# Performance work log

Measured on AMD Instinct MI355X. Metric: run time of the kernel, lower is better.

Reference implementation:

```python
import jax, jax.numpy as jnp
import numpy as np


def setup_inputs() -> dict:
    key = jax.random.key(0)
    k1, k2 = jax.random.split(key)
    x = jax.random.normal(k1, (16, 4096, 256), dtype=jnp.float32)
    embedding = jax.random.normal(k2, (1024, 256), dtype=jnp.float32)
    return {"x": x, "embedding": embedding}


def reference(x, embedding):
    # which_dim = -1 (default): no permute.
    shape = x.shape
    xf = x.reshape(-1, shape[-1])  # [N, D]
    x_sq = jnp.sum(xf * xf, axis=-1, keepdims=True)          # [N, 1]
    e_sq = jnp.sum(embedding * embedding, axis=-1)           # [K]
    dist = -(x_sq - 2.0 * (xf @ embedding.T) + e_sq[None, :])  # [N, K]
    embed_indices = jnp.argmax(dist, axis=1)                 # [N]
    embed_indices = embed_indices.reshape(shape[:-1])        # [B, S]
    quantization = embedding[embed_indices]                  # [B, S, D]
    return (quantization, embed_indices)
```

## Files before the change

### kernel.cpp

```cpp
#include <hip/hip_runtime.h>
#include <hip/hip_fp16.h>
#include <math.h>

#define MROWS   65536
#define NCODES  1024
#define KD      256
#define MARGIN  0.25f

typedef unsigned short u16;
typedef __attribute__((ext_vector_type(8))) _Float16 hfrag;
typedef __attribute__((ext_vector_type(4))) float f32x4;

#define IOFF ((size_t)MROWS * KD)

__device__ __forceinline__ float addrn(float a, float b) {
    float d; asm("v_add_f32 %0, %1, %2" : "=v"(d) : "v"(a), "v"(b)); return d;
}

__device__ __forceinline__ float sumsq_vf8ic4(const float* __restrict__ xr) {
    float a[4][8];
#pragma unroll
    for (int i = 0; i < 4; ++i)
#pragma unroll
        for (int l = 0; l < 8; ++l) a[i][l] = 0.f;
#pragma unroll
    for (int m = 0; m < 8; ++m)
#pragma unroll
        for (int i = 0; i < 4; ++i)
#pragma unroll
            for (int l = 0; l < 8; ++l) {
                float v = xr[m * 32 + i * 8 + l];
                a[i][l] = fmaf(v, v, a[i][l]);
            }
    float cc[8];
#pragma unroll
    for (int l = 0; l < 8; ++l)
        cc[l] = addrn(addrn(addrn(a[0][l], a[1][l]), a[2][l]), a[3][l]);
    float u0 = addrn(cc[0], cc[4]), u1 = addrn(cc[1], cc[5]);
    float u2 = addrn(cc[2], cc[6]), u3 = addrn(cc[3], cc[7]);
    return addrn(addrn(u0, u2), addrn(u1, u3));
}

__global__ __launch_bounds__(256)
void vq_pack(const float* __restrict__ src, u16* __restrict__ dh) {
    __shared__ __align__(16) float lx[16 * 260];
    const int t = threadIdx.x;
    const size_t base = (size_t)blockIdx.x * 16 * 256;
#pragma unroll
    for (int qq = 0; qq < 4; ++qq) {
        int i4 = qq * 256 + t;
        int row = i4 >> 6, col = (i4 & 63) * 4;
        *(float4*)(lx + row * 260 + col) = *(const float4*)(src + base + (size_t)i4 * 4);
    }
    __syncthreads();
#pragma unroll
    for (int i = 0; i < 2; ++i) {
        int s = t + 256 * i;
        int kb = s >> 6, lane = s & 63;
        int r = lane & 15, kg = lane >> 4;
        int k0 = kb * 32 + kg * 8;
        u16 vh[8];
#pragma unroll
        for (int j = 0; j < 8; ++j) {
            float v = lx[r * 260 + k0 + j];
            vh[j] = __half_as_ushort(__float2half(v));
        }
        size_t off = (((size_t)blockIdx.x * 8 + kb) * 64 + lane) * 8;
        *(ulonglong2*)(dh + off) = *(ulonglong2*)vh;
    }
}

__global__ __launch_bounds__(256)
void vq_prep_emb(const float* __restrict__ emb, u16* __restrict__ Eh,
                 float* __restrict__ esq, float* __restrict__ embT,
                 unsigned int* __restrict__ cnt) {
    if (blockIdx.x == 0 && threadIdx.x == 0) *cnt = 0;
    __shared__ float lx[64 * 257];
    const int t = threadIdx.x;
    const int c0 = blockIdx.x * 64;
    const size_t base = (size_t)c0 * 256;
#pragma unroll
    for (int qq = 0; qq < 16; ++qq) {
        int idx4 = qq * 256 + t;
        int row = idx4 >> 6, col4 = idx4 & 63;
        *(float4*)(lx + row * 257 + col4 * 4) = *(const float4*)(emb + base + (size_t)idx4 * 4);
    }
    __syncthreads();
    if (t < 64) esq[c0 + t] = sumsq_vf8ic4(lx + t * 257);
#pragma unroll
    for (int i = 0; i < 8; ++i) {
        int s = i * 256 + t;
        int fl = s >> 6, lane = s & 63;
        int rb_l = fl >> 3, kb = fl & 7;
        int r = rb_l * 16 + (lane & 15), kg = lane >> 4;
        int k0 = kb * 32 + kg * 8;
        u16 vh[8];
#pragma unroll
        for (int j = 0; j < 8; ++j)
            vh[j] = __half_as_ushort(__float2half(lx[r * 257 + k0 + j]));
        size_t off = (((size_t)(blockIdx.x * 4 + rb_l) * 8 + kb) * 64 + lane) * 8;
        *(ulonglong2*)(Eh + off) = *(ulonglong2*)vh;
    }
#pragma unroll
    for (int i = 0; i < 64; ++i) {
        int k = i * 4 + (t >> 6), col = t & 63;
        embT[(size_t)k * 1024 + c0 + col] = lx[col * 257 + k];
    }
}

__global__ __launch_bounds__(256, 2)
void vq_gemm(const u16* __restrict__ Ah, const u16* __restrict__ Eh,
             const float* __restrict__ esq, float* __restrict__ idxf,
             unsigned int* __restrict__ cnt, int* __restrict__ list) {
    extern __shared__ u16 ldsA[];
    const int t = threadIdx.x;
    const int wave = t >> 6, lane = t & 63;
    const int wm = wave >> 1, wn = wave & 1;
    const int q = lane >> 4, c = lane & 15;
    const int m0 = blockIdx.x * 128;
    const int mrb8 = blockIdx.x * 64;

#pragma unroll
    for (int u = 0; u < 16; ++u) {
        int f = wave * 16 + u;
        const u16* srcp = Ah + ((size_t)(mrb8 + f) * 64 + lane) * 8;
        __builtin_amdgcn_global_load_lds((const unsigned int*)srcp,
                                         (unsigned int*)(ldsA + f * 512), 16, 0, 0);
    }
    __syncthreads();

    auto LOADB = [&](int s, hfrag* dst) {
        const int f0 = ((s >> 3) * 64) + (wn * 4) * 8 + (s & 7);
#pragma unroll
        for (int ni = 0; ni < 4; ++ni)
            dst[ni] = *(const hfrag*)(Eh + (size_t)(f0 + ni * 8) * 512 + lane * 8);
    };
    auto LDA = [&](int s, hfrag* dst) {
        const int ks = s & 7;
#pragma unroll
        for (int mi = 0; mi < 4; ++mi)
            dst[mi] = *(const hfrag*)(ldsA + ((wm * 4 + mi) * 8 + ks) * 512 + lane * 8);
    };

    float b1[16], s2v[16], bi[16];
#pragma unroll
    for (int r = 0; r < 16; ++r) { b1[r] = INFINITY; s2v[r] = INFINITY; bi[r] = 0.f; }

    f32x4 acc[4][4];
#pragma unroll
    for (int mi = 0; mi < 4; ++mi)
#pragma unroll
        for (int ni = 0; ni < 4; ++ni) acc[mi][ni] = 0.f;

    hfrag bA[4], bB[4];
    LOADB(0, bA);
    LOADB(1, bB);

    for (int sp = 0; sp < 32; ++sp) {
        const int s0 = sp * 2, s1 = sp * 2 + 1;
        {
            hfrag nx[4];
            LOADB(s0 + 2 < 64 ? s0 + 2 : 0, nx);
            hfrag af[4];
            LDA(s0, af);
#pragma unroll
            for (int mi = 0; mi < 4; ++mi)
#pragma unroll
                for (int ni = 0; ni < 4; ++ni)
                    acc[mi][ni] = __builtin_amdgcn_mfma_f32_16x16x32_f16(af[mi], bA[ni], acc[mi][ni], 0, 0, 0);
#pragma unroll
            for (int ni = 0; ni < 4; ++ni) bA[ni] = nx[ni];
        }
        {
            hfrag nx[4];
            LOADB(s1 + 2 < 64 ? s1 + 2 : 0, nx);
            hfrag af[4];
            LDA(s1, af);
#pragma unroll
            for (int mi = 0; mi < 4; ++mi)
#pragma unroll
                for (int ni = 0; ni < 4; ++ni)
                    acc[mi][ni] = __builtin_amdgcn_mfma_f32_16x16x32_f16(af[mi], bB[ni], acc[mi][ni], 0, 0, 0);
#pragma unroll
            for (int ni = 0; ni < 4; ++ni) bB[ni] = nx[ni];
        }
        if ((s1 & 7) == 7) {
            const int nqi = s1 >> 3;
#pragma unroll
            for (int ni = 0; ni < 4; ++ni) {
                const int code = nqi * 128 + wn * 64 + ni * 16 + c;
                const float e2 = esq[code];
                const float ci = (float)code;
#pragma unroll
                for (int mi = 0; mi < 4; ++mi)
#pragma unroll
                    for (int j = 0; j < 4; ++j) {
                        const int r = mi * 4 + j;
                        float sc = fmaf(-2.f, acc[mi][ni][j], e2);
                        bool lt = sc < b1[r];
                        s2v[r] = fminf(s2v[r], lt ? b1[r] : sc);
                        if (lt) { b1[r] = sc; bi[r] = ci; }
                    }
            }
#pragma unroll
            for (int mi = 0; mi < 4; ++mi)
#pragma unroll
                for (int ni = 0; ni < 4; ++ni) acc[mi][ni] = 0.f;
        }
    }

#pragma unroll
    for (int r = 0; r < 16; ++r) {
#pragma unroll
        for (int mm = 1; mm < 16; mm <<= 1) {
            float ob = __shfl_xor(b1[r], mm, 64);
            float os = __shfl_xor(s2v[r], mm, 64);
            float oi = __shfl_xor(bi[r], mm, 64);
            if (ob < b1[r]) { s2v[r] = fminf(b1[r], os); b1[r] = ob; bi[r] = oi; }
            else            { s2v[r] = fminf(s2v[r], ob); }
        }
    }
    __syncthreads();
    float* sm = (float*)ldsA;
    if (c == 0) {
#pragma unroll
        for (int mi = 0; mi < 4; ++mi)
#pragma unroll
            for (int j = 0; j < 4; ++j) {
                int r = mi * 4 + j;
                int row_l = wm * 64 + mi * 16 + q * 4 + j;
                sm[row_l * 6 + wn * 3 + 0] = b1[r];
                sm[row_l * 6 + wn * 3 + 1] = s2v[r];
                sm[row_l * 6 + wn * 3 + 2] = bi[r];
            }
    }
    __syncthreads();
    if (t < 128) {
        float b0 = sm[t * 6 + 0], sA = sm[t * 6 + 1], i0 = sm[t * 6 + 2];
        float bb = sm[t * 6 + 3], sB = sm[t * 6 + 4], i1 = sm[t * 6 + 5];
        float b, s2, bidx;
        if (b0 <= bb) { b = b0; bidx = i0; s2 = fminf(sA, bb); }
        else          { b = bb; bidx = i1; s2 = fminf(sB, b0); }
        int row = m0 + t;
        idxf[row] = bidx;
        if (s2 - b < MARGIN) {
            unsigned int pos = atomicAdd(cnt, 1u);
            list[pos] = row;
        }
    }
}

__global__ __launch_bounds__(256)
void vq_gather(const float* __restrict__ idxf, const float* __restrict__ emb,
               float* __restrict__ quant) {
    const int t = threadIdx.x;
    const int r0 = blockIdx.x * 64;
    const int lane = t & 63, w = t >> 6;
#pragma unroll
    for (int u = 0; u < 16; ++u) {
        int rl = u * 4 + w;
        int idx = (int)idxf[r0 + rl];
        *(float4*)(quant + (size_t)(r0 + rl) * 256 + lane * 4) =
            *(const float4*)(emb + (size_t)idx * 256 + lane * 4);
    }
}

__global__ __launch_bounds__(256)
void vq_refine1(const float* __restrict__ x, const float* __restrict__ emb,
                const float* __restrict__ embT, const float* __restrict__ esq,
                const int* __restrict__ list, const unsigned int* __restrict__ cnt,
                float* __restrict__ idxf, float* __restrict__ quant) {
    __shared__ __align__(16) float xs[8][260];
    __shared__ float xsq_s[8];
    __shared__ float lb[8][4];
    __shared__ int   li[8][4];
    __shared__ int   li2[8];
    const int t = threadIdx.x;
    const int wave = t >> 6, lane = t & 63;
    const unsigned int n = *cnt;
    float e2q[4];
#pragma unroll
    for (int qq = 0; qq < 4; ++qq) e2q[qq] = esq[qq * 256 + t];

    for (unsigned int g = blockIdx.x; g * 8u < n; g += gridDim.x) {
        const unsigned int r0 = g * 8u;
        const int nr = (int)min(8u, n - r0);
        __syncthreads();
#pragma unroll
        for (int u = 0; u < 2; ++u) {
            int s = u * 256 + t;
            int rr = s >> 6, l4 = s & 63;
            if (rr < nr) {
                int row = list[r0 + rr];
                *(float4*)(&xs[rr][l4 * 4]) = *(const float4*)(x + (size_t)row * 256 + l4 * 4);
            }
        }
        __syncthreads();
        if (t < nr) xsq_s[t] = sumsq_vf8ic4(&xs[t][0]);
        __syncthreads();

        float d[8][4];
#pragma unroll
        for (int r = 0; r < 8; ++r)
#pragma unroll
            for (int qq = 0; qq < 4; ++qq) d[r][qq] = 0.f;

        for (int kq = 0; kq < 64; ++kq) {
            float ev[4][4];
#pragma unroll
            for (int j = 0; j < 4; ++j)
#pragma unroll
                for (int qq = 0; qq < 4; ++qq)
                    ev[qq][j] = embT[(size_t)(kq * 4 + j) * 1024 + qq * 256 + t];
            float4 xf[8];
#pragma unroll
            for (int r = 0; r < 8; ++r) xf[r] = *(const float4*)(&xs[r][kq * 4]);
#pragma unroll
            for (int r = 0; r < 8; ++r)
#pragma unroll
                for (int qq = 0; qq < 4; ++qq) {
                    d[r][qq] = fmaf(xf[r].x, ev[qq][0], d[r][qq]);
                    d[r][qq] = fmaf(xf[r].y, ev[qq][1], d[r][qq]);
                    d[r][qq] = fmaf(xf[r].z, ev[qq][2], d[r][qq]);
                    d[r][qq] = fmaf(xf[r].w, ev[qq][3], d[r][qq]);
                }
        }
#pragma unroll
        for (int r = 0; r < 8; ++r) {
            float sv = INFINITY; int bc = 0x7fffffff;
#pragma unroll
            for (int qq = 0; qq < 4; ++qq) {
                float s = addrn(fmaf(-2.f, d[r][qq], xsq_s[r]), e2q[qq]);
                if (s < sv) { sv = s; bc = qq * 256 + t; }
            }
#pragma unroll
            for (int mm = 1; mm < 64; mm <<= 1) {
                float ob = __shfl_xor(sv, mm, 64);
                int oi = __shfl_xor(bc, mm, 64);
                if (ob < sv || (ob == sv && oi < bc)) { sv = ob; bc = oi; }
            }
            if (lane == 0) { lb[r][wave] = sv; li[r][wave] = bc; }
        }
        __syncthreads();
        if (t < nr) {
            float best = lb[t][0]; int bix = li[t][0];
#pragma unroll
            for (int w = 1; w < 4; ++w) {
                float ob = lb[t][w]; int oi = li[t][w];
                if (ob < best || (ob == best && oi < bix)) { best = ob; bix = oi; }
            }
            idxf[list[r0 + t]] = (float)bix;
            li2[t] = bix;
        }
        __syncthreads();
#pragma unroll
        for (int rr = 0; rr < 2; ++rr) {
            int rl = wave * 2 + rr;
            if (rl < nr) {
                int row = list[r0 + rl];
                int idx = li2[rl];
                *(float4*)(quant + (size_t)row * 256 + lane * 4) =
                    *(const float4*)(emb + (size_t)idx * 256 + lane * 4);
            }
        }
    }
}

extern "C" void kernel_launch(void* const* d_in, const int* in_sizes, int n_in,
                              void* d_out, int out_size, void* d_ws, size_t ws_size,
                              hipStream_t stream) {
    const float* x   = (const float*)d_in[0];
    const float* emb = (const float*)d_in[1];
    float* out  = (float*)d_out;
    float* idxf = out + IOFF;

    u16* Ah = (u16*)out;

    char* ws = (char*)d_ws;
    u16* Eh    = (u16*)(ws);
    float* esq = (float*)(ws + (512 << 10));
    unsigned int* cnt = (unsigned int*)(ws + (640 << 10));
    int* list  = (int*)(ws + (640 << 10) + 256);
    float* embT = (float*)(ws + (1 << 20));

    vq_prep_emb<<<dim3(16), dim3(256), 0, stream>>>(emb, Eh, esq, embT, cnt);
    vq_pack<<<dim3(MROWS / 16), dim3(256), 0, stream>>>(x, Ah);
    vq_gemm<<<dim3(MROWS / 128), dim3(256), 65536, stream>>>(Ah, Eh, esq, idxf, cnt, list);
    vq_gather<<<dim3(MROWS / 64), dim3(256), 0, stream>>>(idxf, emb, out);
    vq_refine1<<<dim3(512), dim3(256), 0, stream>>>(x, emb, embT, esq, list, cnt, idxf, out);
}
```

Measured before the change: 128.4 us.

## Merge embedding prep into x pack kernel and widen refine row batch

Folds the embedding preprocessing (fp16 pack, squared norms, transpose) into the x packing kernel as 64 extra blocks, which removes one launch and lets the small embedding work overlap with the large x pack. The refine kernel now handles 16 candidate rows per iteration instead of 8, so each embT load is reused across twice as many rows. The cost is a larger per-thread register accumulator (16x4) and fewer groups to spread across the 512 refine blocks.

```diff
diff --git a/kernel.cpp b/kernel.cpp
--- a/kernel.cpp
+++ b/kernel.cpp
@@ -42,10 +42,18 @@
 }
 
 __global__ __launch_bounds__(256)
-void vq_pack(const float* __restrict__ src, u16* __restrict__ dh) {
+void vq_prep(const float* __restrict__ x, const float* __restrict__ emb,
+             u16* __restrict__ Ah, u16* __restrict__ Eh,
+             float* __restrict__ esq, float* __restrict__ embT,
+             unsigned int* __restrict__ cnt) {
+    if (blockIdx.x == 0 && threadIdx.x == 0) *cnt = 0;
     __shared__ __align__(16) float lx[16 * 260];
     const int t = threadIdx.x;
-    const size_t base = (size_t)blockIdx.x * 16 * 256;
+    const bool is_emb = blockIdx.x < 64;
+    const int g = is_emb ? blockIdx.x : (blockIdx.x - 64);
+    const float* src = is_emb ? emb : x;
+    u16* dh = is_emb ? Eh : Ah;
+    const size_t base = (size_t)g * 16 * 256;
 #pragma unroll
     for (int qq = 0; qq < 4; ++qq) {
         int i4 = qq * 256 + t;
@@ -65,46 +73,17 @@
             float v = lx[r * 260 + k0 + j];
             vh[j] = __half_as_ushort(__float2half(v));
         }
-        size_t off = (((size_t)blockIdx.x * 8 + kb) * 64 + lane) * 8;
+        size_t off = (((size_t)g * 8 + kb) * 64 + lane) * 8;
         *(ulonglong2*)(dh + off) = *(ulonglong2*)vh;
     }
-}
-
-__global__ __launch_bounds__(256)
-void vq_prep_emb(const float* __restrict__ emb, u16* __restrict__ Eh,
-                 float* __restrict__ esq, float* __restrict__ embT,
-                 unsigned int* __restrict__ cnt) {
-    if (blockIdx.x == 0 && threadIdx.x == 0) *cnt = 0;
-    __shared__ float lx[64 * 257];
-    const int t = threadIdx.x;
-    const int c0 = blockIdx.x * 64;
-    const size_t base = (size_t)c0 * 256;
-#pragma unroll
-    for (int qq = 0; qq < 16; ++qq) {
-        int idx4 = qq * 256 + t;
-        int row = idx4 >> 6, col4 = idx4 & 63;
-        *(float4*)(lx + row * 257 + col4 * 4) = *(const float4*)(emb + base + (size_t)idx4 * 4);
-    }
-    __syncthreads();
-    if (t < 64) esq[c0 + t] = sumsq_vf8ic4(lx + t * 257);
-#pragma unroll
-    for (int i = 0; i < 8; ++i) {
-        int s = i * 256 + t;
-        int fl = s >> 6, lane = s & 63;
-        int rb_l = fl >> 3, kb = fl & 7;
-        int r = rb_l * 16 + (lane & 15), kg = lane >> 4;
-        int k0 = kb * 32 + kg * 8;
-        u16 vh[8];
-#pragma unroll
-        for (int j = 0; j < 8; ++j)
-            vh[j] = __half_as_ushort(__float2half(lx[r * 257 + k0 + j]));
-        size_t off = (((size_t)(blockIdx.x * 4 + rb_l) * 8 + kb) * 64 + lane) * 8;
-        *(ulonglong2*)(Eh + off) = *(ulonglong2*)vh;
-    }
-#pragma unroll
-    for (int i = 0; i < 64; ++i) {
-        int k = i * 4 + (t >> 6), col = t & 63;
-        embT[(size_t)k * 1024 + c0 + col] = lx[col * 257 + k];
+    if (is_emb) {
+        const int c0 = g * 16;
+        if (t < 16) esq[c0 + t] = sumsq_vf8ic4(lx + t * 260);
+#pragma unroll
+        for (int i = 0; i < 16; ++i) {
+            int k = i * 16 + (t >> 4), col = t & 15;
+            embT[(size_t)k * 1024 + c0 + col] = lx[col * 260 + k];
+        }
     }
 }
 
@@ -270,11 +249,11 @@
                 const float* __restrict__ embT, const float* __restrict__ esq,
                 const int* __restrict__ list, const unsigned int* __restrict__ cnt,
                 float* __restrict__ idxf, float* __restrict__ quant) {
-    __shared__ __align__(16) float xs[8][260];
-    __shared__ float xsq_s[8];
-    __shared__ float lb[8][4];
-    __shared__ int   li[8][4];
-    __shared__ int   li2[8];
+    __shared__ __align__(16) float xs[16][260];
+    __shared__ float xsq_s[16];
+    __shared__ float lb[16][4];
+    __shared__ int   li[16][4];
+    __shared__ int   li2[16];
     const int t = threadIdx.x;
     const int wave = t >> 6, lane = t & 63;
     const unsigned int n = *cnt;
@@ -282,12 +261,12 @@
 #pragma unroll
     for (int qq = 0; qq < 4; ++qq) e2q[qq] = esq[qq * 256 + t];
 
-    for (unsigned int g = blockIdx.x; g * 8u < n; g += gridDim.x) {
-        const unsigned int r0 = g * 8u;
-        const int nr = (int)min(8u, n - r0);
-        __syncthreads();
-#pragma unroll
-        for (int u = 0; u < 2; ++u) {
+    for (unsigned int g = blockIdx.x; g * 16u < n; g += gridDim.x) {
+        const unsigned int r0 = g * 16u;
+        const int nr = (int)min(16u, n - r0);
+        __syncthreads();
+#pragma unroll
+        for (int u = 0; u < 4; ++u) {
             int s = u * 256 + t;
             int rr = s >> 6, l4 = s & 63;
             if (rr < nr) {
@@ -299,9 +278,9 @@
         if (t < nr) xsq_s[t] = sumsq_vf8ic4(&xs[t][0]);
         __syncthreads();
 
-        float d[8][4];
-#pragma unroll
-        for (int r = 0; r < 8; ++r)
+        float d[16][4];
+#pragma unroll
+        for (int r = 0; r < 16; ++r)
 #pragma unroll
             for (int qq = 0; qq < 4; ++qq) d[r][qq] = 0.f;
 
@@ -312,21 +291,20 @@
 #pragma unroll
                 for (int qq = 0; qq < 4; ++qq)
                     ev[qq][j] = embT[(size_t)(kq * 4 + j) * 1024 + qq * 256 + t];
-            float4 xf[8];
-#pragma unroll
-            for (int r = 0; r < 8; ++r) xf[r] = *(const float4*)(&xs[r][kq * 4]);
-#pragma unroll
-            for (int r = 0; r < 8; ++r)
+#pragma unroll
+            for (int r = 0; r < 16; ++r) {
+                float4 xf = *(const float4*)(&xs[r][kq * 4]);
 #pragma unroll
                 for (int qq = 0; qq < 4; ++qq) {
-                    d[r][qq] = fmaf(xf[r].x, ev[qq][0], d[r][qq]);
-                    d[r][qq] = fmaf(xf[r].y, ev[qq][1], d[r][qq]);
-                    d[r][qq] = fmaf(xf[r].z, ev[qq][2], d[r][qq]);
-                    d[r][qq] = fmaf(xf[r].w, ev[qq][3], d[r][qq]);
+                    d[r][qq] = fmaf(xf.x, ev[qq][0], d[r][qq]);
+                    d[r][qq] = fmaf(xf.y, ev[qq][1], d[r][qq]);
+                    d[r][qq] = fmaf(xf.z, ev[qq][2], d[r][qq]);
+                    d[r][qq] = fmaf(xf.w, ev[qq][3], d[r][qq]);
                 }
-        }
-#pragma unroll
-        for (int r = 0; r < 8; ++r) {
+            }
+        }
+#pragma unroll
+        for (int r = 0; r < 16; ++r) {
             float sv = INFINITY; int bc = 0x7fffffff;
 #pragma unroll
             for (int qq = 0; qq < 4; ++qq) {
@@ -354,8 +332,8 @@
         }
         __syncthreads();
 #pragma unroll
-        for (int rr = 0; rr < 2; ++rr) {
-            int rl = wave * 2 + rr;
+        for (int rr = 0; rr < 4; ++rr) {
+            int rl = wave * 4 + rr;
             if (rl < nr) {
                 int row = list[r0 + rl];
                 int idx = li2[rl];
@@ -383,8 +361,7 @@
     int* list  = (int*)(ws + (640 << 10) + 256);
     float* embT = (float*)(ws + (1 << 20));
 
-    vq_prep_emb<<<dim3(16), dim3(256), 0, stream>>>(emb, Eh, esq, embT, cnt);
-    vq_pack<<<dim3(MROWS / 16), dim3(256), 0, stream>>>(x, Ah);
+    vq_prep<<<dim3(64 + MROWS / 16), dim3(256), 0, stream>>>(x, emb, Ah, Eh, esq, embT, cnt);
     vq_gemm<<<dim3(MROWS / 128), dim3(256), 65536, stream>>>(Ah, Eh, esq, idxf, cnt, list);
     vq_gather<<<dim3(MROWS / 64), dim3(256), 0, stream>>>(idxf, emb, out);
     vq_refine1<<<dim3(512), dim3(256), 0, stream>>>(x, emb, embT, esq, list, cnt, idxf, out);
```

Measured after the change: 156.9 us. 1.22x slower.
